# Optimization experiments

Hardware: AMD Instinct MI355X
Metric: run time of the kernel (lower is better)

Reference implementation:

```python
import jax, jax.numpy as jnp
import numpy as np

T, DIM, E, INTER, TOPK = 4096, 1024, 8, 1408, 2


def setup_inputs() -> dict:
    key = jax.random.key(0)
    k_x, k_idx, k1, k2, k3 = jax.random.split(key, 5)
    scale = 1.0 / np.sqrt(DIM)
    return {
        "x": jax.random.normal(k_x, (T, DIM), dtype=jnp.float32),
        "expert_indices": jax.random.randint(k_idx, (T, TOPK), 0, E, dtype=jnp.int64),
        "w1": jax.random.normal(k1, (E, INTER, DIM), dtype=jnp.float32) * scale,
        "w2": jax.random.normal(k2, (E, DIM, INTER), dtype=jnp.float32) * scale,
        "w3": jax.random.normal(k3, (E, INTER, DIM), dtype=jnp.float32) * scale,
    }


def reference(x, expert_indices, w1, w2, w3):
    # All-expert SwiGLU FFN: [T, E, INTER]
    x1 = jax.nn.silu(jnp.einsum('ti,eoi->teo', x, w1))
    x3 = jnp.einsum('ti,eoi->teo', x, w3)
    # Down-projection per expert: [T, E, DIM]
    expert_outs = jnp.einsum('teo,eio->tei', x1 * x3, w2)
    # Gather only the routed experts per token: [T, TOPK, DIM]
    return jnp.take_along_axis(expert_outs, expert_indices[:, :, None], axis=1)
```

## Files before the change

### kernel.cpp

```cpp
#include <hip/hip_runtime.h>

#define TTOK   4096
#define DIMK   1024
#define NEXP   8
#define INTERN 1408
#define NPAIRS 8192

#define BM  128
#define BN  128
#define BK  64
#define NTH 256
#define MAXRT (NPAIRS / BM + NEXP - 1)
#define NT1  (INTERN / BN)
#define NT2  (DIMK / BN)

typedef __attribute__((ext_vector_type(8))) _Float16 half8;
typedef __attribute__((ext_vector_type(4))) float f32x4;

#define MFMAF16(a, b, c) __builtin_amdgcn_mfma_f32_16x16x32_f16((a), (b), (c), 0, 0, 0)

__device__ __forceinline__ void gl_lds16(const void* g, void* l) {
  __builtin_amdgcn_global_load_lds(
      (const __attribute__((address_space(1))) void*)g,
      (__attribute__((address_space(3))) void*)l, 16, 0, 0);
}

__device__ __forceinline__ int xcd_swz(int orig, int G) {
  int q = G >> 3, r = G & 7, x = orig & 7, p = orig >> 3;
  return (x < r ? x * (q + 1) : r * (q + 1) + (x - r) * q) + p;
}

__global__ __launch_bounds__(NTH) void convert_kernel(
    const float* __restrict__ src, unsigned short* __restrict__ dst, int n4) {
  int i = blockIdx.x * blockDim.x + threadIdx.x;
  const int stride = gridDim.x * blockDim.x;
  for (; i < n4; i += stride) {
    float4 v = reinterpret_cast<const float4*>(src)[i];
    ushort4 o;
    o.x = __builtin_bit_cast(unsigned short, (_Float16)v.x);
    o.y = __builtin_bit_cast(unsigned short, (_Float16)v.y);
    o.z = __builtin_bit_cast(unsigned short, (_Float16)v.z);
    o.w = __builtin_bit_cast(unsigned short, (_Float16)v.w);
    reinterpret_cast<ushort4*>(dst)[i] = o;
  }
}

__global__ void route_kernel(const int* __restrict__ w, int* __restrict__ offs,
                             int* __restrict__ pairs) {
  __shared__ int cnt[NEXP], base[NEXP], cur[NEXP], mode;
  const int t = threadIdx.x;
  if (t == 0) mode = 0;
  if (t < NEXP) cnt[t] = 0;
  __syncthreads();
  int any = 0;
  for (int i = t; i < NPAIRS / 2; i += NTH) any |= w[2 * i + 1];
  if (any) atomicOr(&mode, 1);
  __syncthreads();
  const int m32 = mode;
  for (int i = t; i < NPAIRS; i += NTH) {
    int e = (m32 ? w[i] : w[2 * i]) & (NEXP - 1);
    atomicAdd(&cnt[e], 1);
  }
  __syncthreads();
  if (t == 0) {
    int s = 0;
    for (int e = 0; e < NEXP; ++e) { base[e] = s; offs[e] = s; s += cnt[e]; }
    offs[NEXP] = s;
  }
  __syncthreads();
  if (t < NEXP) cur[t] = base[t];
  __syncthreads();
  for (int i = t; i < NPAIRS; i += NTH) {
    int e = (m32 ? w[i] : w[2 * i]) & (NEXP - 1);
    int p = atomicAdd(&cur[e], 1);
    pairs[p] = i;
  }
}

__device__ __forceinline__ bool find_tile(const int* __restrict__ offs, int rt,
                                          int &e, int &row0, int &row_end) {
  int cum = 0;
  for (int i = 0; i < NEXP; ++i) {
    int b = offs[i], en = offs[i + 1];
    int nt = (en - b + BM - 1) / BM;
    if (rt < cum + nt) { e = i; row0 = b + (rt - cum) * BM; row_end = en; return true; }
    cum += nt;
  }
  return false;
}

__global__ __launch_bounds__(NTH, 2) void gemm1_kernel(
    const unsigned short* __restrict__ xf, const unsigned short* __restrict__ w1f,
    const unsigned short* __restrict__ w3f, const int* __restrict__ offs,
    const int* __restrict__ pairs, unsigned short* __restrict__ hf) {
  __shared__ __align__(16) unsigned short At[BM * BK];
  __shared__ __align__(16) unsigned short B1t[BN * BK];
  __shared__ __align__(16) unsigned short B3t[BN * BK];

  const int lid = xcd_swz((int)blockIdx.x, MAXRT * NT1);
  const int rt = lid % MAXRT, nt = lid / MAXRT;
  int e, row0, row_end;
  if (!find_tile(offs, rt, e, row0, row_end)) return;
  const int n0 = nt * BN;
  const int t = threadIdx.x;
  const int ln = t & 63;
  const int wv = t >> 6;
  const int wm = wv >> 1, wn = wv & 1;
  const int fr = ln & 15, fg = ln >> 4;
  const int sr = ln >> 3, sc = ln & 7;
  const int sw = (sc ^ sr) * 8;

  size_t aA[4], aB[4];
#pragma unroll
  for (int c = 0; c < 4; ++c) {
    int row = wv * 32 + c * 8 + sr;
    int p = row0 + row;
    int tok = ((p < row_end) ? pairs[p] : pairs[row0]) >> 1;
    aA[c] = (size_t)tok * DIMK + sw;
    aB[c] = ((size_t)e * INTERN + n0 + row) * DIMK + sw;
  }

  f32x4 acc1[4][4] = {};
  f32x4 acc3[4][4] = {};

  for (int k0 = 0; k0 < DIMK; k0 += BK) {
#pragma unroll
    for (int c = 0; c < 4; ++c)
      gl_lds16(xf + aA[c] + k0, &At[(wv * 32 + c * 8) * BK]);
#pragma unroll
    for (int c = 0; c < 4; ++c)
      gl_lds16(w1f + aB[c] + k0, &B1t[(wv * 32 + c * 8) * BK]);
#pragma unroll
    for (int c = 0; c < 4; ++c)
      gl_lds16(w3f + aB[c] + k0, &B3t[(wv * 32 + c * 8) * BK]);
    __syncthreads();

#pragma unroll
    for (int kk = 0; kk < 2; ++kk) {
      half8 ah[4];
#pragma unroll
      for (int m = 0; m < 4; ++m) {
        int row = wm * 64 + m * 16 + fr;
        ah[m] = *reinterpret_cast<const half8*>(
            &At[row * BK + (((kk * 4 + fg) ^ (fr & 7)) * 8)]);
      }
#pragma unroll
      for (int n = 0; n < 4; ++n) {
        int row = wn * 64 + n * 16 + fr;
        int bo = row * BK + (((kk * 4 + fg) ^ (fr & 7)) * 8);
        half8 b1 = *reinterpret_cast<const half8*>(&B1t[bo]);
        half8 b3 = *reinterpret_cast<const half8*>(&B3t[bo]);
#pragma unroll
        for (int m = 0; m < 4; ++m) {
          acc1[m][n] = MFMAF16(ah[m], b1, acc1[m][n]);
          acc3[m][n] = MFMAF16(ah[m], b3, acc3[m][n]);
        }
      }
    }
    __syncthreads();
  }

#pragma unroll
  for (int m = 0; m < 4; ++m)
#pragma unroll
    for (int n = 0; n < 4; ++n)
#pragma unroll
      for (int r = 0; r < 4; ++r) {
        int p = row0 + wm * 64 + m * 16 + fg * 4 + r;
        if (p < row_end) {
          int col = n0 + wn * 64 + n * 16 + fr;
          float a1 = acc1[m][n][r], a3 = acc3[m][n][r];
          float hv = (a1 / (1.0f + __expf(-a1))) * a3;
          hf[(size_t)p * INTERN + col] =
              __builtin_bit_cast(unsigned short, (_Float16)hv);
        }
      }
}

__global__ __launch_bounds__(NTH, 2) void gemm2_kernel(
    const unsigned short* __restrict__ w2f, const int* __restrict__ offs,
    const int* __restrict__ pairs, const unsigned short* __restrict__ hf,
    float* __restrict__ out) {
  __shared__ __align__(16) unsigned short At[BM * BK];
  __shared__ __align__(16) unsigned short Bt[BN * BK];

  const int lid = xcd_swz((int)blockIdx.x, MAXRT * NT2);
  const int rt = lid % MAXRT, nt = lid / MAXRT;
  int e, row0, row_end;
  if (!find_tile(offs, rt, e, row0, row_end)) return;
  const int n0 = nt * BN;
  const int t = threadIdx.x;
  const int ln = t & 63;
  const int wv = t >> 6;
  const int wm = wv >> 1, wn = wv & 1;
  const int fr = ln & 15, fg = ln >> 4;
  const int sr = ln >> 3, sc = ln & 7;
  const int sw = (sc ^ sr) * 8;

  size_t aA[4], aB[4];
#pragma unroll
  for (int c = 0; c < 4; ++c) {
    int row = wv * 32 + c * 8 + sr;
    int p = row0 + row;
    int ar = (p < row_end) ? p : row0;
    aA[c] = (size_t)ar * INTERN + sw;
    aB[c] = ((size_t)e * DIMK + n0 + row) * INTERN + sw;
  }

  f32x4 acc[4][4] = {};

  for (int k0 = 0; k0 < INTERN; k0 += BK) {
#pragma unroll
    for (int c = 0; c < 4; ++c)
      gl_lds16(hf + aA[c] + k0, &At[(wv * 32 + c * 8) * BK]);
#pragma unroll
    for (int c = 0; c < 4; ++c)
      gl_lds16(w2f + aB[c] + k0, &Bt[(wv * 32 + c * 8) * BK]);
    __syncthreads();

#pragma unroll
    for (int kk = 0; kk < 2; ++kk) {
      half8 ah[4];
#pragma unroll
      for (int m = 0; m < 4; ++m) {
        int row = wm * 64 + m * 16 + fr;
        ah[m] = *reinterpret_cast<const half8*>(
            &At[row * BK + (((kk * 4 + fg) ^ (fr & 7)) * 8)]);
      }
#pragma unroll
      for (int n = 0; n < 4; ++n) {
        int row = wn * 64 + n * 16 + fr;
        half8 b = *reinterpret_cast<const half8*>(
            &Bt[row * BK + (((kk * 4 + fg) ^ (fr & 7)) * 8)]);
#pragma unroll
        for (int m = 0; m < 4; ++m)
          acc[m][n] = MFMAF16(ah[m], b, acc[m][n]);
      }
    }
    __syncthreads();
  }

#pragma unroll
  for (int m = 0; m < 4; ++m)
#pragma unroll
    for (int n = 0; n < 4; ++n)
#pragma unroll
      for (int r = 0; r < 4; ++r) {
        int p = row0 + wm * 64 + m * 16 + fg * 4 + r;
        if (p < row_end) {
          int orow = pairs[p];
          out[(size_t)orow * DIMK + n0 + wn * 64 + n * 16 + fr] = acc[m][n][r];
        }
      }
}

extern "C" void kernel_launch(void* const* d_in, const int* in_sizes, int n_in,
                              void* d_out, int out_size, void* d_ws, size_t ws_size,
                              hipStream_t stream) {
  const float* x  = (const float*)d_in[0];
  const int*   ei = (const int*)d_in[1];
  const float* w1 = (const float*)d_in[2];
  const float* w2 = (const float*)d_in[3];
  const float* w3 = (const float*)d_in[4];
  float* out = (float*)d_out;

  char* ws = (char*)d_ws;
  int* offs  = (int*)ws;
  int* pairs = (int*)(ws + 256);

  const size_t sz_x = (size_t)TTOK * DIMK;
  const size_t sz_w = (size_t)NEXP * INTERN * DIMK;
  const size_t sz_h = (size_t)NPAIRS * INTERN;
  size_t off = 65536;
  unsigned short* x_f  = (unsigned short*)(ws + off); off += sz_x * 2;
  unsigned short* w1_f = (unsigned short*)(ws + off); off += sz_w * 2;
  unsigned short* w3_f = (unsigned short*)(ws + off); off += sz_w * 2;
  unsigned short* w2_f = (unsigned short*)(ws + off); off += sz_w * 2;
  unsigned short* h_f  = (unsigned short*)(ws + off);

  route_kernel<<<1, NTH, 0, stream>>>(ei, offs, pairs);
  convert_kernel<<<2048, NTH, 0, stream>>>(x,  x_f,  (int)(sz_x / 4));
  convert_kernel<<<2048, NTH, 0, stream>>>(w1, w1_f, (int)(sz_w / 4));
  convert_kernel<<<2048, NTH, 0, stream>>>(w3, w3_f, (int)(sz_w / 4));
  convert_kernel<<<2048, NTH, 0, stream>>>(w2, w2_f, (int)(sz_w / 4));
  gemm1_kernel<<<MAXRT * NT1, NTH, 0, stream>>>(x_f, w1_f, w3_f, offs, pairs, h_f);
  gemm2_kernel<<<MAXRT * NT2, NTH, 0, stream>>>(w2_f, offs, pairs, h_f, out);
}
```

Measured before the change: 312.7 us.

## Use 8-wave GEMM blocks and fuse fp16 conversions into one kernel

Both grouped GEMM kernels now run 512 threads (8 waves) per 128x128 tile, each wave computing a 64x32 subtile, with launch bounds targeting 4 blocks per CU to raise wave occupancy and latency hiding. The four separate fp32->fp16 conversion launches are merged into a single kernel that dispatches by index range. The risk is tighter register budget, more LDS A-fragment reads per block and larger barrier cost with more waves.

```diff
diff --git a/kernel.cpp b/kernel.cpp
--- a/kernel.cpp
+++ b/kernel.cpp
@@ -10,6 +10,7 @@
 #define BN  128
 #define BK  64
 #define NTH 256
+#define NTG 512
 #define MAXRT (NPAIRS / BM + NEXP - 1)
 #define NT1  (INTERN / BN)
 #define NT2  (DIMK / BN)
@@ -30,18 +31,29 @@
   return (x < r ? x * (q + 1) : r * (q + 1) + (x - r) * q) + p;
 }
 
-__global__ __launch_bounds__(NTH) void convert_kernel(
-    const float* __restrict__ src, unsigned short* __restrict__ dst, int n4) {
+#define N4X (TTOK * DIMK / 4)
+#define N4W (NEXP * INTERN * DIMK / 4)
+__global__ __launch_bounds__(NTH) void convert_all_kernel(
+    const float* __restrict__ x, const float* __restrict__ w1,
+    const float* __restrict__ w3, const float* __restrict__ w2,
+    unsigned short* __restrict__ xf, unsigned short* __restrict__ w1f,
+    unsigned short* __restrict__ w3f, unsigned short* __restrict__ w2f) {
+  const int total = N4X + 3 * N4W;
   int i = blockIdx.x * blockDim.x + threadIdx.x;
   const int stride = gridDim.x * blockDim.x;
-  for (; i < n4; i += stride) {
-    float4 v = reinterpret_cast<const float4*>(src)[i];
+  for (; i < total; i += stride) {
+    const float* src; unsigned short* dst; int j;
+    if (i < N4X) { src = x; dst = xf; j = i; }
+    else if (i < N4X + N4W) { src = w1; dst = w1f; j = i - N4X; }
+    else if (i < N4X + 2 * N4W) { src = w3; dst = w3f; j = i - N4X - N4W; }
+    else { src = w2; dst = w2f; j = i - N4X - 2 * N4W; }
+    float4 v = reinterpret_cast<const float4*>(src)[j];
     ushort4 o;
     o.x = __builtin_bit_cast(unsigned short, (_Float16)v.x);
     o.y = __builtin_bit_cast(unsigned short, (_Float16)v.y);
     o.z = __builtin_bit_cast(unsigned short, (_Float16)v.z);
     o.w = __builtin_bit_cast(unsigned short, (_Float16)v.w);
-    reinterpret_cast<ushort4*>(dst)[i] = o;
+    reinterpret_cast<ushort4*>(dst)[j] = o;
   }
 }
 
@@ -89,7 +101,7 @@
   return false;
 }
 
-__global__ __launch_bounds__(NTH, 2) void gemm1_kernel(
+__global__ __launch_bounds__(NTG, 4) void gemm1_kernel(
     const unsigned short* __restrict__ xf, const unsigned short* __restrict__ w1f,
     const unsigned short* __restrict__ w3f, const int* __restrict__ offs,
     const int* __restrict__ pairs, unsigned short* __restrict__ hf) {
@@ -105,34 +117,34 @@
   const int t = threadIdx.x;
   const int ln = t & 63;
   const int wv = t >> 6;
-  const int wm = wv >> 1, wn = wv & 1;
+  const int wm = wv >> 2, wn = wv & 3;
   const int fr = ln & 15, fg = ln >> 4;
   const int sr = ln >> 3, sc = ln & 7;
   const int sw = (sc ^ sr) * 8;
 
-  size_t aA[4], aB[4];
-#pragma unroll
-  for (int c = 0; c < 4; ++c) {
-    int row = wv * 32 + c * 8 + sr;
+  size_t aA[2], aB[2];
+#pragma unroll
+  for (int c = 0; c < 2; ++c) {
+    int row = wv * 16 + c * 8 + sr;
     int p = row0 + row;
     int tok = ((p < row_end) ? pairs[p] : pairs[row0]) >> 1;
     aA[c] = (size_t)tok * DIMK + sw;
     aB[c] = ((size_t)e * INTERN + n0 + row) * DIMK + sw;
   }
 
-  f32x4 acc1[4][4] = {};
-  f32x4 acc3[4][4] = {};
+  f32x4 acc1[4][2] = {};
+  f32x4 acc3[4][2] = {};
 
   for (int k0 = 0; k0 < DIMK; k0 += BK) {
 #pragma unroll
-    for (int c = 0; c < 4; ++c)
-      gl_lds16(xf + aA[c] + k0, &At[(wv * 32 + c * 8) * BK]);
-#pragma unroll
-    for (int c = 0; c < 4; ++c)
-      gl_lds16(w1f + aB[c] + k0, &B1t[(wv * 32 + c * 8) * BK]);
-#pragma unroll
-    for (int c = 0; c < 4; ++c)
-      gl_lds16(w3f + aB[c] + k0, &B3t[(wv * 32 + c * 8) * BK]);
+    for (int c = 0; c < 2; ++c)
+      gl_lds16(xf + aA[c] + k0, &At[(wv * 16 + c * 8) * BK]);
+#pragma unroll
+    for (int c = 0; c < 2; ++c)
+      gl_lds16(w1f + aB[c] + k0, &B1t[(wv * 16 + c * 8) * BK]);
+#pragma unroll
+    for (int c = 0; c < 2; ++c)
+      gl_lds16(w3f + aB[c] + k0, &B3t[(wv * 16 + c * 8) * BK]);
     __syncthreads();
 
 #pragma unroll
@@ -145,8 +157,8 @@
             &At[row * BK + (((kk * 4 + fg) ^ (fr & 7)) * 8)]);
       }
 #pragma unroll
-      for (int n = 0; n < 4; ++n) {
-        int row = wn * 64 + n * 16 + fr;
+      for (int n = 0; n < 2; ++n) {
+        int row = wn * 32 + n * 16 + fr;
         int bo = row * BK + (((kk * 4 + fg) ^ (fr & 7)) * 8);
         half8 b1 = *reinterpret_cast<const half8*>(&B1t[bo]);
         half8 b3 = *reinterpret_cast<const half8*>(&B3t[bo]);
@@ -163,12 +175,12 @@
 #pragma unroll
   for (int m = 0; m < 4; ++m)
 #pragma unroll
-    for (int n = 0; n < 4; ++n)
+    for (int n = 0; n < 2; ++n)
 #pragma unroll
       for (int r = 0; r < 4; ++r) {
         int p = row0 + wm * 64 + m * 16 + fg * 4 + r;
         if (p < row_end) {
-          int col = n0 + wn * 64 + n * 16 + fr;
+          int col = n0 + wn * 32 + n * 16 + fr;
           float a1 = acc1[m][n][r], a3 = acc3[m][n][r];
           float hv = (a1 / (1.0f + __expf(-a1))) * a3;
           hf[(size_t)p * INTERN + col] =
@@ -177,7 +189,7 @@
       }
 }
 
-__global__ __launch_bounds__(NTH, 2) void gemm2_kernel(
+__global__ __launch_bounds__(NTG, 4) void gemm2_kernel(
     const unsigned short* __restrict__ w2f, const int* __restrict__ offs,
     const int* __restrict__ pairs, const unsigned short* __restrict__ hf,
     float* __restrict__ out) {
@@ -192,30 +204,30 @@
   const int t = threadIdx.x;
   const int ln = t & 63;
   const int wv = t >> 6;
-  const int wm = wv >> 1, wn = wv & 1;
+  const int wm = wv >> 2, wn = wv & 3;
   const int fr = ln & 15, fg = ln >> 4;
   const int sr = ln >> 3, sc = ln & 7;
   const int sw = (sc ^ sr) * 8;
 
-  size_t aA[4], aB[4];
-#pragma unroll
-  for (int c = 0; c < 4; ++c) {
-    int row = wv * 32 + c * 8 + sr;
+  size_t aA[2], aB[2];
+#pragma unroll
+  for (int c = 0; c < 2; ++c) {
+    int row = wv * 16 + c * 8 + sr;
     int p = row0 + row;
     int ar = (p < row_end) ? p : row0;
     aA[c] = (size_t)ar * INTERN + sw;
     aB[c] = ((size_t)e * DIMK + n0 + row) * INTERN + sw;
   }
 
-  f32x4 acc[4][4] = {};
+  f32x4 acc[4][2] = {};
 
   for (int k0 = 0; k0 < INTERN; k0 += BK) {
 #pragma unroll
-    for (int c = 0; c < 4; ++c)
-      gl_lds16(hf + aA[c] + k0, &At[(wv * 32 + c * 8) * BK]);
-#pragma unroll
-    for (int c = 0; c < 4; ++c)
-      gl_lds16(w2f + aB[c] + k0, &Bt[(wv * 32 + c * 8) * BK]);
+    for (int c = 0; c < 2; ++c)
+      gl_lds16(hf + aA[c] + k0, &At[(wv * 16 + c * 8) * BK]);
+#pragma unroll
+    for (int c = 0; c < 2; ++c)
+      gl_lds16(w2f + aB[c] + k0, &Bt[(wv * 16 + c * 8) * BK]);
     __syncthreads();
 
 #pragma unroll
@@ -228,8 +240,8 @@
             &At[row * BK + (((kk * 4 + fg) ^ (fr & 7)) * 8)]);
       }
 #pragma unroll
-      for (int n = 0; n < 4; ++n) {
-        int row = wn * 64 + n * 16 + fr;
+      for (int n = 0; n < 2; ++n) {
+        int row = wn * 32 + n * 16 + fr;
         half8 b = *reinterpret_cast<const half8*>(
             &Bt[row * BK + (((kk * 4 + fg) ^ (fr & 7)) * 8)]);
 #pragma unroll
@@ -243,13 +255,13 @@
 #pragma unroll
   for (int m = 0; m < 4; ++m)
 #pragma unroll
-    for (int n = 0; n < 4; ++n)
+    for (int n = 0; n < 2; ++n)
 #pragma unroll
       for (int r = 0; r < 4; ++r) {
         int p = row0 + wm * 64 + m * 16 + fg * 4 + r;
         if (p < row_end) {
           int orow = pairs[p];
-          out[(size_t)orow * DIMK + n0 + wn * 64 + n * 16 + fr] = acc[m][n][r];
+          out[(size_t)orow * DIMK + n0 + wn * 32 + n * 16 + fr] = acc[m][n][r];
         }
       }
 }
@@ -270,7 +282,6 @@
 
   const size_t sz_x = (size_t)TTOK * DIMK;
   const size_t sz_w = (size_t)NEXP * INTERN * DIMK;
-  const size_t sz_h = (size_t)NPAIRS * INTERN;
   size_t off = 65536;
   unsigned short* x_f  = (unsigned short*)(ws + off); off += sz_x * 2;
   unsigned short* w1_f = (unsigned short*)(ws + off); off += sz_w * 2;
@@ -279,10 +290,7 @@
   unsigned short* h_f  = (unsigned short*)(ws + off);
 
   route_kernel<<<1, NTH, 0, stream>>>(ei, offs, pairs);
-  convert_kernel<<<2048, NTH, 0, stream>>>(x,  x_f,  (int)(sz_x / 4));
-  convert_kernel<<<2048, NTH, 0, stream>>>(w1, w1_f, (int)(sz_w / 4));
-  convert_kernel<<<2048, NTH, 0, stream>>>(w3, w3_f, (int)(sz_w / 4));
-  convert_kernel<<<2048, NTH, 0, stream>>>(w2, w2_f, (int)(sz_w / 4));
-  gemm1_kernel<<<MAXRT * NT1, NTH, 0, stream>>>(x_f, w1_f, w3_f, offs, pairs, h_f);
-  gemm2_kernel<<<MAXRT * NT2, NTH, 0, stream>>>(w2_f, offs, pairs, h_f, out);
-}
+  convert_all_kernel<<<4096, NTH, 0, stream>>>(x, w1, w3, w2, x_f, w1_f, w3_f, w2_f);
+  gemm1_kernel<<<MAXRT * NT1, NTG, 0, stream>>>(x_f, w1_f, w3_f, offs, pairs, h_f);
+  gemm2_kernel<<<MAXRT * NT2, NTG, 0, stream>>>(w2_f, offs, pairs, h_f, out);
+}
```

Result: no change. 307.2 us (-1.8%).
